# Kernel optimization log

Measured on AMD Instinct MI355X. Metric: run time of the kernel, lower is better.

The kernel has to match this reference:

```python
import jax, jax.numpy as jnp
import numpy as np

ALPHA = 10.0
BETA = 2.0


def _l2norm(x):
    return x / jnp.linalg.norm(x, axis=1, keepdims=True)


def setup_inputs() -> dict:
    key = jax.random.key(0)
    k1, k2, k3 = jax.random.split(key, 3)
    n, C, d = 4096, 10000, 2048
    inputs = _l2norm(jax.random.normal(k1, (n, d), dtype=jnp.float32))
    kernel = _l2norm(jax.random.normal(k2, (C, d), dtype=jnp.float32))
    targets = jax.random.randint(k3, (n,), 0, C, dtype=jnp.int64 if jax.config.jax_enable_x64 else jnp.int32)
    return {"inputs": inputs, "targets": targets, "kernel": kernel}


def reference(inputs, targets, kernel):
    n = inputs.shape[0]
    C = kernel.shape[0]
    rows = jnp.arange(n)

    # cos_theta uses a detached kernel (no grad through this GEMM in original)
    cos = jnp.clip(inputs @ jax.lax.stop_gradient(kernel).T, -1.0, 1.0)  # [n, C]

    # phi_i = <inputs_i, kernel[targets_i]> - beta  (grad flows to kernel here)
    phi = jnp.sum(inputs * kernel[targets], axis=1) - BETA  # [n]

    pos_cos = cos[rows, targets]  # cos_theta at target columns, [n]
    mean_proxy_pos = pos_cos.sum() / n
    mean_proxy_neg = (cos.sum() - pos_cos.sum()) / (n * (C - 1))

    # output = cos_theta with target entries replaced by phi
    output = cos.at[rows, targets].set(phi)  # [n, C]
    onehot = jax.nn.one_hot(targets, C, dtype=output.dtype)

    loss_pos = phi  # sum(output * onehot, axis=1)
    loss_neg = jnp.log(jnp.sum(jnp.exp(output * ALPHA) * (1.0 - onehot), axis=1))  # [n]
    loss_mask = (jnp.max(output, axis=1) - phi) > 0.0
    per_sample = -loss_pos + loss_neg / ALPHA
    denom = jnp.maximum(loss_mask.sum(), 1).astype(per_sample.dtype)
    loss = jnp.sum(jnp.where(loss_mask, per_sample, 0.0)) / denom

    pred = jnp.argmax(output, axis=1)
    prec = jnp.mean((pred == targets).astype(jnp.float32))

    sim = inputs @ inputs.T  # [n, n]
    sim_label = (targets[:, None] == targets[None, :]).astype(sim.dtype)
    pos_cnt = sim_label.sum()
    neg_cnt = (n * n) - pos_cnt
    mean_pos_sim = jnp.sum(sim * sim_label) / pos_cnt
    mean_neg_sim = jnp.sum(sim * (1.0 - sim_label)) / neg_cnt

    return (loss, prec, mean_proxy_pos, mean_proxy_neg, mean_pos_sim, mean_neg_sim)
```

## Files before the change

### kernel.cpp

```cpp
#include <hip/hip_runtime.h>
#include <hip/hip_bf16.h>

#define NROWS 4096
#define NCLS  10000
#define DIM   2048
#define DIMB  1024
#define ALPHA_F 10.0f
#define BETA_F  2.0f
#define FP4_SCALE 64.0f
#define INVQ (1.0f / (FP4_SCALE * FP4_SCALE))
#define NMAIN_BLK 2560
#define NSIM_BLK  528

typedef float f32x4 __attribute__((ext_vector_type(4)));
typedef int   i32x4 __attribute__((ext_vector_type(4)));
typedef int   i32x8 __attribute__((ext_vector_type(8)));

__global__ void cast_fp4_kernel(const float* __restrict__ X, const float* __restrict__ Kn,
                                unsigned int* __restrict__ dA, unsigned int* __restrict__ dB,
                                int nA8, int nT8) {
  int stride = gridDim.x * blockDim.x;
  for (int i = blockIdx.x * blockDim.x + threadIdx.x; i < nT8; i += stride) {
    const float* src; unsigned int* dst; int j;
    if (i < nA8) { src = X; dst = dA; j = i; } else { src = Kn; dst = dB; j = i - nA8; }
    float4 a = reinterpret_cast<const float4*>(src)[2 * j];
    float4 b = reinterpret_cast<const float4*>(src)[2 * j + 1];
    float v[8] = {a.x, a.y, a.z, a.w, b.x, b.y, b.z, b.w};
    unsigned int w = 0;
#pragma unroll
    for (int q = 0; q < 8; ++q) {
      float s = v[q] * FP4_SCALE;
      float av = fabsf(s);
      unsigned int code = (unsigned)(av > 0.25f) + (av > 0.75f) + (av > 1.25f)
                        + (av > 1.75f) + (av > 2.5f) + (av > 3.5f) + (av > 5.0f);
      code |= (s < 0.f) ? 8u : 0u;
      w |= code << (4 * q);
    }
    dst[j] = w;
  }
}

__global__ void gather_dot_kernel(const float* __restrict__ X, const float* __restrict__ Kn,
                                  const int* __restrict__ tgt, float* __restrict__ dotv) {
  int gtid = blockIdx.x * blockDim.x + threadIdx.x;
  int wave = gtid >> 6;
  int lane = threadIdx.x & 63;
  if (wave >= NROWS) return;
  const float* xr = X + (size_t)wave * DIM;
  const float* kr = Kn + (size_t)tgt[wave] * DIM;
  float s = 0.f;
#pragma unroll
  for (int it = 0; it < DIM / 256; ++it) {
    int k = lane * 4 + it * 256;
    float4 a = *reinterpret_cast<const float4*>(xr + k);
    float4 b = *reinterpret_cast<const float4*>(kr + k);
    s += a.x * b.x + a.y * b.y + a.z * b.z + a.w * b.w;
  }
#pragma unroll
  for (int off = 32; off > 0; off >>= 1) s += __shfl_down(s, off);
  if (lane == 0) dotv[wave] = s;
}


#define AS1 const __attribute__((address_space(1))) void*
#define AS3 __attribute__((address_space(3))) void*

__global__ __launch_bounds__(256, 4)
void gemm_kernel(const unsigned char* __restrict__ A,
                 const unsigned char* __restrict__ Bm,
                 const float* __restrict__ dotv,
                 const int* __restrict__ tgt,
                 float* __restrict__ S1, float* __restrict__ Eacc,
                 float* __restrict__ CNT, float* __restrict__ simAcc) {
  __shared__ unsigned char lds[2 * 16384];

  const int tid  = threadIdx.x;
  const int lane = tid & 63;
  const int wid  = tid >> 6;
  const int wr   = wid >> 1;
  const int wc   = wid & 1;
  const int fr   = lane & 15;
  const int kg   = lane >> 4;

  const int lin = blockIdx.x;
  const bool isMain = lin < NMAIN_BLK;
  int rowTile, colTile, nB;
  const unsigned char* B;
  if (isMain) {
    int swz = (lin & 7) * 320 + (lin >> 3);
    colTile = swz / 32;
    rowTile = swz % 32;
    B = Bm; nB = NCLS;
  } else {
    int l2 = lin - NMAIN_BLK;
    int swz = (l2 & 7) * 66 + (l2 >> 3);
    int r = 0;
    while ((r + 1) * (r + 2) / 2 <= swz) ++r;
    rowTile = r;
    colTile = swz - r * (r + 1) / 2;
    B = A; nB = NROWS;
  }
  const int rowBase = rowTile * 128;
  const int colBase = colTile * 128;

  const int l0  = tid >> 3;
  const int sp  = tid & 7;
  const int lg8 = sp ^ (l0 & 7);
  const int shi = lg8 >> 2, sc16 = lg8 & 3;
  const int rA0 = rowBase + 2 * l0 + shi;
  const int rA1 = rA0 + 64;
  int cB0 = colBase + 2 * l0 + shi;      if (cB0 > nB - 1) cB0 = nB - 1;
  int cB1 = colBase + 64 + 2 * l0 + shi; if (cB1 > nB - 1) cB1 = nB - 1;
  const unsigned char* pA0 = A + (size_t)rA0 * DIMB + sc16 * 16;
  const unsigned char* pA1 = A + (size_t)rA1 * DIMB + sc16 * 16;
  const unsigned char* pB0 = B + (size_t)cB0 * DIMB + sc16 * 16;
  const unsigned char* pB1 = B + (size_t)cB1 * DIMB + sc16 * 16;
  const int dOff = l0 * 128 + sp * 16;

#define STAGE_TILE(BUF, KT)                                                     \
  { int ko_ = (KT) * 64;                                                        \
    unsigned char* d_ = lds + (BUF) * 16384 + dOff;                             \
    __builtin_amdgcn_global_load_lds((AS1)(pA0 + ko_), (AS3)(d_),          16, 0, 0); \
    __builtin_amdgcn_global_load_lds((AS1)(pA1 + ko_), (AS3)(d_ + 4096),   16, 0, 0); \
    __builtin_amdgcn_global_load_lds((AS1)(pB0 + ko_), (AS3)(d_ + 8192),   16, 0, 0); \
    __builtin_amdgcn_global_load_lds((AS1)(pB1 + ko_), (AS3)(d_ + 12288),  16, 0, 0); }

  int offA[4], offB[4];
#pragma unroll
  for (int m2 = 0; m2 < 4; ++m2) {
    int lr = wr * 64 + m2 * 16 + fr;
    int l = lr >> 1;
    offA[m2] = l * 128 + ((((lr & 1) * 4 + kg) ^ (l & 7)) << 4);
  }
#pragma unroll
  for (int n2 = 0; n2 < 4; ++n2) {
    int lc = wc * 64 + n2 * 16 + fr;
    int l = lc >> 1;
    offB[n2] = 8192 + l * 128 + ((((lc & 1) * 4 + kg) ^ (l & 7)) << 4);
  }

  f32x4 acc[4][4];
  const f32x4 zero = {0.f, 0.f, 0.f, 0.f};
#pragma unroll
  for (int m = 0; m < 4; ++m)
#pragma unroll
    for (int n = 0; n < 4; ++n) acc[m][n] = zero;

  STAGE_TILE(0, 0);
  __syncthreads();

#pragma unroll 1
  for (int kt = 0; kt < 16; ++kt) {
    const int buf = kt & 1;
    const int ktn = (kt < 15) ? kt + 1 : 15;
    STAGE_TILE(buf ^ 1, ktn);
    const unsigned char* lb = lds + buf * 16384;
    i32x8 afr[4], bfr[4];
#pragma unroll
    for (int m2 = 0; m2 < 4; ++m2) {
      i32x4 v_ = *reinterpret_cast<const i32x4*>(lb + offA[m2]);
      afr[m2][0] = v_[0]; afr[m2][1] = v_[1]; afr[m2][2] = v_[2]; afr[m2][3] = v_[3];
      afr[m2][4] = 0; afr[m2][5] = 0; afr[m2][6] = 0; afr[m2][7] = 0;
    }
#pragma unroll
    for (int n2 = 0; n2 < 4; ++n2) {
      i32x4 v_ = *reinterpret_cast<const i32x4*>(lb + offB[n2]);
      bfr[n2][0] = v_[0]; bfr[n2][1] = v_[1]; bfr[n2][2] = v_[2]; bfr[n2][3] = v_[3];
      bfr[n2][4] = 0; bfr[n2][5] = 0; bfr[n2][6] = 0; bfr[n2][7] = 0;
    }
    __builtin_amdgcn_s_setprio(1);
#pragma unroll
    for (int m2 = 0; m2 < 4; ++m2)
#pragma unroll
      for (int n2 = 0; n2 < 4; ++n2)
        acc[m2][n2] = __builtin_amdgcn_mfma_scale_f32_16x16x128_f8f6f4(
            afr[m2], bfr[n2], acc[m2][n2], 4, 4, 0, 127, 0, 127);
    __builtin_amdgcn_s_setprio(0);
    __syncthreads();
  }

  __syncthreads();

  if (isMain) {
    float* shPhi = reinterpret_cast<float*>(lds);
    if (tid < 128) shPhi[tid] = dotv[rowBase + tid] - BETA_F;
    __syncthreads();
#pragma unroll
    for (int m = 0; m < 4; ++m) {
#pragma unroll
      for (int j = 0; j < 4; ++j) {
        int rl = wr * 64 + m * 16 + kg * 4 + j;
        float ph = shPhi[rl];
        float s1 = 0.f, ee = 0.f, ct = 0.f;
#pragma unroll
        for (int n = 0; n < 4; ++n) {
          int gcol = colBase + wc * 64 + n * 16 + fr;
          float c = acc[m][n][j] * INVQ;
          c = fminf(fmaxf(c, -1.f), 1.f);
          if (gcol < NCLS) {
            s1 += c;
            ee += __expf(ALPHA_F * c);
            ct += (c > ph) ? 1.f : 0.f;
          }
        }
#pragma unroll
        for (int o = 1; o < 16; o <<= 1) {
          s1 += __shfl_xor(s1, o);
          ee += __shfl_xor(ee, o);
          ct += __shfl_xor(ct, o);
        }
        if (fr == 0) {
          int grow = rowBase + rl;
          atomicAdd(&S1[grow], s1);
          atomicAdd(&Eacc[grow], ee);
          atomicAdd(&CNT[grow], ct);
        }
      }
    }
  } else {
    const float wgt = (rowTile == colTile) ? 1.f : 2.f;
    int* shT = reinterpret_cast<int*>(lds);
    float* redbuf = reinterpret_cast<float*>(lds + 4096);
    if (tid < 128) shT[tid] = tgt[rowBase + tid];
    else if (tid < 256) shT[tid] = tgt[colBase + (tid - 128)];
    __syncthreads();
    float ps = 0.f, als = 0.f, pc = 0.f;
#pragma unroll
    for (int m = 0; m < 4; ++m) {
#pragma unroll
      for (int j = 0; j < 4; ++j) {
        int rl = wr * 64 + m * 16 + kg * 4 + j;
        int tr = shT[rl];
#pragma unroll
        for (int n = 0; n < 4; ++n) {
          int cl = wc * 64 + n * 16 + fr;
          float c = acc[m][n][j] * INVQ;
          als += c;
          if (tr == shT[128 + cl]) { ps += c; pc += 1.f; }
        }
      }
    }
#pragma unroll
    for (int o = 1; o < 64; o <<= 1) {
      ps  += __shfl_xor(ps, o);
      als += __shfl_xor(als, o);
      pc  += __shfl_xor(pc, o);
    }
    if (lane == 0) {
      redbuf[wid * 3 + 0] = ps;
      redbuf[wid * 3 + 1] = als;
      redbuf[wid * 3 + 2] = pc;
    }
    __syncthreads();
    if (tid == 0) {
      float p = 0.f, a = 0.f, c2 = 0.f;
      for (int w = 0; w < 4; ++w) {
        p += redbuf[w * 3 + 0];
        a += redbuf[w * 3 + 1];
        c2 += redbuf[w * 3 + 2];
      }
      atomicAdd(&simAcc[0], wgt * p);
      atomicAdd(&simAcc[1], wgt * a);
      atomicAdd(&simAcc[2], wgt * c2);
    }
  }
}

__global__ void finalize_kernel(const float* __restrict__ dotv, const float* __restrict__ S1,
                                const float* __restrict__ Eacc, const float* __restrict__ CNT,
                                const float* __restrict__ simAcc, float* __restrict__ out) {
  __shared__ float sh[5][256];
  int tid = threadIdx.x;
  float sum_posc = 0.f, sum_s1 = 0.f, loss_sum = 0.f, mask_cnt = 0.f, correct = 0.f;
  for (int i = tid; i < NROWS; i += 256) {
    float d = dotv[i];
    float posc = fminf(fmaxf(d, -1.f), 1.f);
    float phi = d - BETA_F;
    sum_posc += posc;
    sum_s1 += S1[i];
    float e = Eacc[i] - __expf(ALPHA_F * posc);
    float cexcl = CNT[i] - 1.f;
    float per = -phi + __logf(e) / ALPHA_F;
    if (cexcl > 0.5f) { loss_sum += per; mask_cnt += 1.f; }
    else correct += 1.f;
  }
  sh[0][tid] = sum_posc; sh[1][tid] = sum_s1; sh[2][tid] = loss_sum;
  sh[3][tid] = mask_cnt; sh[4][tid] = correct;
  __syncthreads();
  for (int s = 128; s > 0; s >>= 1) {
    if (tid < s)
      for (int q = 0; q < 5; ++q) sh[q][tid] += sh[q][tid + s];
    __syncthreads();
  }
  if (tid == 0) {
    float posS = sh[0][0], s1S = sh[1][0], lossS = sh[2][0], maskS = sh[3][0], corr = sh[4][0];
    out[0] = lossS / fmaxf(maskS, 1.f);
    out[1] = corr / (float)NROWS;
    out[2] = posS / (float)NROWS;
    out[3] = (s1S - posS) / ((float)NROWS * (float)(NCLS - 1));
    float pos = simAcc[0], all = simAcc[1], pcnt = simAcc[2];
    out[4] = pos / pcnt;
    out[5] = (all - pos) / ((float)NROWS * (float)NROWS - pcnt);
  }
}

extern "C" void kernel_launch(void* const* d_in, const int* in_sizes, int n_in,
                              void* d_out, int out_size, void* d_ws, size_t ws_size,
                              hipStream_t stream) {
  const float* X  = (const float*)d_in[0];
  const int*   tg = (const int*)d_in[1];
  const float* Kn = (const float*)d_in[2];
  float* out = (float*)d_out;

  char* w = (char*)d_ws;
  unsigned char* f4A = (unsigned char*)w;
  unsigned char* f4B = f4A + (size_t)NROWS * DIMB;
  float* dotv   = (float*)(w + (size_t)NROWS * DIMB + (size_t)NCLS * DIMB);
  float* S1     = dotv + NROWS;
  float* Eacc   = S1 + NROWS;
  float* CNT    = Eacc + NROWS;
  float* simAcc = CNT + NROWS;

  hipMemsetAsync(S1, 0, (3 * NROWS + 4) * sizeof(float), stream);

  const int nA8 = NROWS * DIM / 8, nT8 = nA8 + NCLS * DIM / 8;
  cast_fp4_kernel<<<2048, 256, 0, stream>>>(X, Kn, (unsigned int*)f4A,
                                            (unsigned int*)f4B, nA8, nT8);
  gather_dot_kernel<<<NROWS / 4, 256, 0, stream>>>(X, Kn, tg, dotv);

  gemm_kernel<<<NMAIN_BLK + NSIM_BLK, 256, 0, stream>>>(
      f4A, f4B, dotv, tg, S1, Eacc, CNT, simAcc);

  finalize_kernel<<<1, 256, 0, stream>>>(dotv, S1, Eacc, CNT, simAcc, out);
}
```

Before: 149.2 us.

## Triple-buffer GEMM LDS pipeline and merge cast and gather-dot kernels

```diff
diff --git a/kernel.cpp b/kernel.cpp
--- a/kernel.cpp
+++ b/kernel.cpp
@@ -16,63 +16,63 @@
 typedef int   i32x4 __attribute__((ext_vector_type(4)));
 typedef int   i32x8 __attribute__((ext_vector_type(8)));
 
-__global__ void cast_fp4_kernel(const float* __restrict__ X, const float* __restrict__ Kn,
-                                unsigned int* __restrict__ dA, unsigned int* __restrict__ dB,
-                                int nA8, int nT8) {
-  int stride = gridDim.x * blockDim.x;
-  for (int i = blockIdx.x * blockDim.x + threadIdx.x; i < nT8; i += stride) {
-    const float* src; unsigned int* dst; int j;
-    if (i < nA8) { src = X; dst = dA; j = i; } else { src = Kn; dst = dB; j = i - nA8; }
-    float4 a = reinterpret_cast<const float4*>(src)[2 * j];
-    float4 b = reinterpret_cast<const float4*>(src)[2 * j + 1];
-    float v[8] = {a.x, a.y, a.z, a.w, b.x, b.y, b.z, b.w};
-    unsigned int w = 0;
-#pragma unroll
-    for (int q = 0; q < 8; ++q) {
-      float s = v[q] * FP4_SCALE;
-      float av = fabsf(s);
-      unsigned int code = (unsigned)(av > 0.25f) + (av > 0.75f) + (av > 1.25f)
-                        + (av > 1.75f) + (av > 2.5f) + (av > 3.5f) + (av > 5.0f);
-      code |= (s < 0.f) ? 8u : 0u;
-      w |= code << (4 * q);
-    }
-    dst[j] = w;
-  }
-}
-
-__global__ void gather_dot_kernel(const float* __restrict__ X, const float* __restrict__ Kn,
-                                  const int* __restrict__ tgt, float* __restrict__ dotv) {
-  int gtid = blockIdx.x * blockDim.x + threadIdx.x;
-  int wave = gtid >> 6;
-  int lane = threadIdx.x & 63;
-  if (wave >= NROWS) return;
-  const float* xr = X + (size_t)wave * DIM;
-  const float* kr = Kn + (size_t)tgt[wave] * DIM;
-  float s = 0.f;
-#pragma unroll
-  for (int it = 0; it < DIM / 256; ++it) {
-    int k = lane * 4 + it * 256;
-    float4 a = *reinterpret_cast<const float4*>(xr + k);
-    float4 b = *reinterpret_cast<const float4*>(kr + k);
-    s += a.x * b.x + a.y * b.y + a.z * b.z + a.w * b.w;
-  }
-#pragma unroll
-  for (int off = 32; off > 0; off >>= 1) s += __shfl_down(s, off);
-  if (lane == 0) dotv[wave] = s;
+__global__ void prep_kernel(const float* __restrict__ X, const float* __restrict__ Kn,
+                            const int* __restrict__ tgt,
+                            unsigned int* __restrict__ dA, unsigned int* __restrict__ dB,
+                            float* __restrict__ dotv, int nA8, int nT8) {
+  if (blockIdx.x < 2048) {
+    int stride = 2048 * blockDim.x;
+    for (int i = blockIdx.x * blockDim.x + threadIdx.x; i < nT8; i += stride) {
+      const float* src; unsigned int* dst; int j;
+      if (i < nA8) { src = X; dst = dA; j = i; } else { src = Kn; dst = dB; j = i - nA8; }
+      float4 a = reinterpret_cast<const float4*>(src)[2 * j];
+      float4 b = reinterpret_cast<const float4*>(src)[2 * j + 1];
+      float v[8] = {a.x, a.y, a.z, a.w, b.x, b.y, b.z, b.w};
+      unsigned int w = 0;
+#pragma unroll
+      for (int q = 0; q < 8; ++q) {
+        float s = v[q] * FP4_SCALE;
+        float av = fabsf(s);
+        unsigned int code = (unsigned)(av > 0.25f) + (av > 0.75f) + (av > 1.25f)
+                          + (av > 1.75f) + (av > 2.5f) + (av > 3.5f) + (av > 5.0f);
+        code |= (s < 0.f) ? 8u : 0u;
+        w |= code << (4 * q);
+      }
+      dst[j] = w;
+    }
+  } else {
+    int gtid = (blockIdx.x - 2048) * blockDim.x + threadIdx.x;
+    int wave = gtid >> 6;
+    int lane = threadIdx.x & 63;
+    if (wave >= NROWS) return;
+    const float* xr = X + (size_t)wave * DIM;
+    const float* kr = Kn + (size_t)tgt[wave] * DIM;
+    float s = 0.f;
+#pragma unroll
+    for (int it = 0; it < DIM / 256; ++it) {
+      int k = lane * 4 + it * 256;
+      float4 a = *reinterpret_cast<const float4*>(xr + k);
+      float4 b = *reinterpret_cast<const float4*>(kr + k);
+      s += a.x * b.x + a.y * b.y + a.z * b.z + a.w * b.w;
+    }
+#pragma unroll
+    for (int off = 32; off > 0; off >>= 1) s += __shfl_down(s, off);
+    if (lane == 0) dotv[wave] = s;
+  }
 }
 
 
 #define AS1 const __attribute__((address_space(1))) void*
 #define AS3 __attribute__((address_space(3))) void*
 
-__global__ __launch_bounds__(256, 4)
+__global__ __launch_bounds__(256, 3)
 void gemm_kernel(const unsigned char* __restrict__ A,
                  const unsigned char* __restrict__ Bm,
                  const float* __restrict__ dotv,
                  const int* __restrict__ tgt,
                  float* __restrict__ S1, float* __restrict__ Eacc,
                  float* __restrict__ CNT, float* __restrict__ simAcc) {
-  __shared__ unsigned char lds[2 * 16384];
+  __shared__ unsigned char lds[3 * 16384];
 
   const int tid  = threadIdx.x;
   const int lane = tid & 63;
@@ -147,13 +147,16 @@
     for (int n = 0; n < 4; ++n) acc[m][n] = zero;
 
   STAGE_TILE(0, 0);
-  __syncthreads();
+  STAGE_TILE(1, 1);
+  asm volatile("s_waitcnt vmcnt(4)" ::: "memory");
+  asm volatile("s_barrier" ::: "memory");
 
 #pragma unroll 1
   for (int kt = 0; kt < 16; ++kt) {
-    const int buf = kt & 1;
-    const int ktn = (kt < 15) ? kt + 1 : 15;
-    STAGE_TILE(buf ^ 1, ktn);
+    const int buf = kt % 3;
+    const int sbuf = (kt + 2) % 3;
+    int ktn = kt + 2; if (ktn > 15) ktn = 15;
+    STAGE_TILE(sbuf, ktn);
     const unsigned char* lb = lds + buf * 16384;
     i32x8 afr[4], bfr[4];
 #pragma unroll
@@ -176,9 +179,11 @@
         acc[m2][n2] = __builtin_amdgcn_mfma_scale_f32_16x16x128_f8f6f4(
             afr[m2], bfr[n2], acc[m2][n2], 4, 4, 0, 127, 0, 127);
     __builtin_amdgcn_s_setprio(0);
-    __syncthreads();
-  }
-
+    asm volatile("s_waitcnt vmcnt(4)" ::: "memory");
+    asm volatile("s_barrier" ::: "memory");
+  }
+
+  asm volatile("s_waitcnt vmcnt(0) lgkmcnt(0)" ::: "memory");
   __syncthreads();
 
   if (isMain) {
@@ -324,9 +329,8 @@
   hipMemsetAsync(S1, 0, (3 * NROWS + 4) * sizeof(float), stream);
 
   const int nA8 = NROWS * DIM / 8, nT8 = nA8 + NCLS * DIM / 8;
-  cast_fp4_kernel<<<2048, 256, 0, stream>>>(X, Kn, (unsigned int*)f4A,
-                                            (unsigned int*)f4B, nA8, nT8);
-  gather_dot_kernel<<<NROWS / 4, 256, 0, stream>>>(X, Kn, tg, dotv);
+  prep_kernel<<<3072, 256, 0, stream>>>(X, Kn, tg, (unsigned int*)f4A,
+                                        (unsigned int*)f4B, dotv, nA8, nT8);
 
   gemm_kernel<<<NMAIN_BLK + NSIM_BLK, 256, 0, stream>>>(
       f4A, f4B, dotv, tg, S1, Eacc, CNT, simAcc);
```

Result: no change. 147.3 us (-1.3%).
